# Optimization experiments

Hardware: AMD Instinct MI355X
Metric: run time of the kernel (lower is better)

The kernel has to match this reference:

```python
import jax, jax.numpy as jnp
from jax import lax
import numpy as np

VOCAB, EMB, HID, B, T = 500, 64, 64, 512, 512


def setup_inputs() -> dict:
    key = jax.random.key(0)
    ks = jax.random.split(key, 12)
    s_ih = 1.0 / np.sqrt(HID)
    emb = jax.random.normal(ks[0], (VOCAB, EMB), dtype=jnp.float32)
    emb = emb.at[0].set(0.0)  # padding_idx=0 row is zero-initialized
    u = lambda k, shape: jax.random.uniform(k, shape, jnp.float32, -s_ih, s_ih)
    return {
        "x": jax.random.randint(ks[1], (B, T), 0, VOCAB, dtype=jnp.int64),
        "emb": emb,
        "W_ih0": u(ks[2], (HID, EMB)), "W_hh0": u(ks[3], (HID, HID)),
        "b_ih0": u(ks[4], (HID,)),     "b_hh0": u(ks[5], (HID,)),
        "W_ih1": u(ks[6], (HID, HID)), "W_hh1": u(ks[7], (HID, HID)),
        "b_ih1": u(ks[8], (HID,)),     "b_hh1": u(ks[9], (HID,)),
        "fc_w": u(ks[10], (1, HID)),   "fc_b": u(ks[11], (1,)),
    }


def reference(x, emb, W_ih0, W_hh0, b_ih0, b_hh0, W_ih1, W_hh1, b_ih1, b_hh1, fc_w, fc_b):
    e = emb[x]                                        # [B,T,EMB]
    # Layer-0 input projection is time-parallel; precompute as one big GEMM.
    xin0 = jnp.einsum('bte,he->bth', e, W_ih0) + b_ih0  # [B,T,HID]

    def step(carry, xt):
        h1, h2 = carry
        h1 = jnp.tanh(xt + h1 @ W_hh0.T + b_hh0)
        h2 = jnp.tanh(h1 @ W_ih1.T + b_ih1 + h2 @ W_hh1.T + b_hh1)
        return (h1, h2), None

    h0 = jnp.zeros((x.shape[0], HID), dtype=e.dtype)
    (h1, h2), _ = lax.scan(step, (h0, h0), jnp.swapaxes(xin0, 0, 1))  # scan over T
    return h2 @ fc_w.T + fc_b                          # [B,1]
```

## Files before the change

### kernel.cpp

```cpp
#include <hip/hip_runtime.h>
#include <math.h>

#define VOCAB 500
#define EMB   64
#define HID   64
#define BB    512
#define TT    512

__device__ __forceinline__ float fast_tanh(float x) {
    float ax = fabsf(x);
    float e  = __expf(-2.0f * ax);
    float r  = __builtin_amdgcn_rcpf(1.0f + e);
    float t  = fmaf(-2.0f * e, r, 1.0f);
    return copysignf(t, x);
}

__global__ __launch_bounds__(64) void proj_kernel(
        const float* __restrict__ emb,
        const float* __restrict__ W_ih0,
        const float* __restrict__ b_ih0,
        float* __restrict__ proj) {
    const int v = blockIdx.x;
    const int j = threadIdx.x;
    const float4* e4 = (const float4*)(emb + v * EMB);
    const float4* w4 = (const float4*)(W_ih0 + j * EMB);
    float acc = b_ih0[j];
    #pragma unroll
    for (int k = 0; k < EMB / 4; ++k) {
        float4 e = e4[k];
        float4 w = w4[k];
        acc = fmaf(w.x, e.x, acc);
        acc = fmaf(w.y, e.y, acc);
        acc = fmaf(w.z, e.z, acc);
        acc = fmaf(w.w, e.w, acc);
    }
    proj[v * HID + j] = acc;
}

__global__ __launch_bounds__(192, 1) void rnn_kernel(
        const int*   __restrict__ x,
        const float* __restrict__ proj,
        const float* __restrict__ W_hh0,
        const float* __restrict__ b_hh0,
        const float* __restrict__ W_ih1,
        const float* __restrict__ W_hh1,
        const float* __restrict__ b_ih1,
        const float* __restrict__ b_hh1,
        const float* __restrict__ fc_w,
        const float* __restrict__ fc_b,
        float* __restrict__ out) {
    const int b   = blockIdx.x;
    const int tid = threadIdx.x;
    const int wid = tid >> 6;
    const int j   = tid & 63;

    __shared__ __align__(16) float H1[2][HID];
    __shared__ __align__(16) float H2[2][HID];
    __shared__ __align__(16) float AA[2][HID];
    __shared__ int xls[TT];

    for (int t = tid; t < TT; t += 192) xls[t] = x[b * TT + t];

    const float* wsrc = (wid == 0 ? W_hh0 : (wid == 1 ? W_ih1 : W_hh1)) + j * HID;
    float w[HID];
    {
        const float4* w4 = (const float4*)wsrc;
        #pragma unroll
        for (int k = 0; k < HID / 4; ++k) {
            float4 t4 = w4[k];
            w[4*k+0] = t4.x; w[4*k+1] = t4.y; w[4*k+2] = t4.z; w[4*k+3] = t4.w;
        }
    }
    #pragma unroll
    for (int k = 0; k < HID; ++k) asm volatile("" : "+v"(w[k]));

    const float bh0 = b_hh0[j];
    const float bi1 = b_ih1[j] + b_hh1[j];
    const float fcw = fc_w[j];

    if (tid < HID) {
        H1[0][tid] = 0.0f; H1[1][tid] = 0.0f;
        H2[0][tid] = 0.0f; H2[1][tid] = 0.0f;
    }
    __syncthreads();

    float xin = (wid == 0) ? proj[xls[0] * HID + j] : 0.0f;
    float h2n = 0.0f;

    for (int p = 0; p < TT + 2; ++p) {
        const int cur = p & 1;
        const int prv = cur ^ 1;

        if (wid == 0) {
            if (p < TT) {
                const int   idxn = xls[(p + 1) & (TT - 1)];
                const float xinn = proj[idxn * HID + j];

                const float4* h = (const float4*)H1[prv];
                float p0 = xin + bh0, p1 = 0.0f, p2 = 0.0f, p3 = 0.0f;
                #pragma unroll
                for (int k = 0; k < HID / 4; ++k) {
                    float4 hv = h[k];
                    p0 = fmaf(w[4*k+0], hv.x, p0);
                    p1 = fmaf(w[4*k+1], hv.y, p1);
                    p2 = fmaf(w[4*k+2], hv.z, p2);
                    p3 = fmaf(w[4*k+3], hv.w, p3);
                }
                H1[cur][j] = fast_tanh((p0 + p1) + (p2 + p3));
                xin = xinn;
            }
        } else if (wid == 1) {
            if (p >= 1 && p <= TT) {
                const float4* h = (const float4*)H1[prv];
                float p0 = 0.0f, p1 = 0.0f, p2 = 0.0f, p3 = 0.0f;
                #pragma unroll
                for (int k = 0; k < HID / 4; ++k) {
                    float4 hv = h[k];
                    p0 = fmaf(w[4*k+0], hv.x, p0);
                    p1 = fmaf(w[4*k+1], hv.y, p1);
                    p2 = fmaf(w[4*k+2], hv.z, p2);
                    p3 = fmaf(w[4*k+3], hv.w, p3);
                }
                AA[prv][j] = (p0 + p1) + (p2 + p3);
            }
        } else {
            if (p >= 2) {
                const float4* h = (const float4*)H2[prv];
                float p0 = bi1 + AA[cur][j], p1 = 0.0f, p2 = 0.0f, p3 = 0.0f;
                #pragma unroll
                for (int k = 0; k < HID / 4; ++k) {
                    float4 hv = h[k];
                    p0 = fmaf(w[4*k+0], hv.x, p0);
                    p1 = fmaf(w[4*k+1], hv.y, p1);
                    p2 = fmaf(w[4*k+2], hv.z, p2);
                    p3 = fmaf(w[4*k+3], hv.w, p3);
                }
                h2n = fast_tanh((p0 + p1) + (p2 + p3));
                H2[cur][j] = h2n;
            }
        }
        __syncthreads();
    }

    if (wid == 2) {
        float val = h2n * fcw;
        #pragma unroll
        for (int o = 32; o > 0; o >>= 1) val += __shfl_down(val, o, 64);
        if (j == 0) out[b] = val + fc_b[0];
    }
}

extern "C" void kernel_launch(void* const* d_in, const int* in_sizes, int n_in,
                              void* d_out, int out_size, void* d_ws, size_t ws_size,
                              hipStream_t stream) {
    const int*   x     = (const int*)  d_in[0];
    const float* emb   = (const float*)d_in[1];
    const float* W_ih0 = (const float*)d_in[2];
    const float* W_hh0 = (const float*)d_in[3];
    const float* b_ih0 = (const float*)d_in[4];
    const float* b_hh0 = (const float*)d_in[5];
    const float* W_ih1 = (const float*)d_in[6];
    const float* W_hh1 = (const float*)d_in[7];
    const float* b_ih1 = (const float*)d_in[8];
    const float* b_hh1 = (const float*)d_in[9];
    const float* fc_w  = (const float*)d_in[10];
    const float* fc_b  = (const float*)d_in[11];
    float* out  = (float*)d_out;
    float* proj = (float*)d_ws;

    proj_kernel<<<VOCAB, 64, 0, stream>>>(emb, W_ih0, b_ih0, proj);
    rnn_kernel<<<BB, 192, 0, stream>>>(x, proj, W_hh0, b_hh0,
                                       W_ih1, W_hh1, b_ih1, b_hh1,
                                       fc_w, fc_b, out);
}
```

Baseline: 323.2 us.

## Chunk recurrence by 8 steps with readlane broadcasts to cut block barriers

Each wave now handles 8 timesteps per barrier instead of one. The two recurrent waves keep their hidden state in a register and broadcast it with readlane rather than reading it back from shared memory. Layer-1 input products pass through chunked double-buffered shared arrays. This cuts __syncthreads from one per timestep to one per chunk and removes LDS round-trips on the serial critical path. In exchange it uses 64 scalar readlanes per step and adds a longer pipeline fill across the three waves.

```diff
diff --git a/kernel.cpp b/kernel.cpp
--- a/kernel.cpp
+++ b/kernel.cpp
@@ -6,6 +6,8 @@
 #define HID   64
 #define BB    512
 #define TT    512
+#define KC    8
+#define NC    (TT / KC)
 
 __device__ __forceinline__ float fast_tanh(float x) {
     float ax = fabsf(x);
@@ -13,6 +15,10 @@
     float r  = __builtin_amdgcn_rcpf(1.0f + e);
     float t  = fmaf(-2.0f * e, r, 1.0f);
     return copysignf(t, x);
+}
+
+__device__ __forceinline__ float bcast(float v, int lane) {
+    return __int_as_float(__builtin_amdgcn_readlane(__float_as_int(v), lane));
 }
 
 __global__ __launch_bounds__(64) void proj_kernel(
@@ -54,9 +60,8 @@
     const int wid = tid >> 6;
     const int j   = tid & 63;
 
-    __shared__ __align__(16) float H1[2][HID];
-    __shared__ __align__(16) float H2[2][HID];
-    __shared__ __align__(16) float AA[2][HID];
+    __shared__ __align__(16) float H1R[2][KC][HID];
+    __shared__ __align__(16) float AAR[2][KC][HID];
     __shared__ int xls[TT];
 
     for (int t = tid; t < TT; t += 192) xls[t] = x[b * TT + t];
@@ -78,72 +83,78 @@
     const float bi1 = b_ih1[j] + b_hh1[j];
     const float fcw = fc_w[j];
 
-    if (tid < HID) {
-        H1[0][tid] = 0.0f; H1[1][tid] = 0.0f;
-        H2[0][tid] = 0.0f; H2[1][tid] = 0.0f;
-    }
     __syncthreads();
 
-    float xin = (wid == 0) ? proj[xls[0] * HID + j] : 0.0f;
-    float h2n = 0.0f;
+    float h1reg = 0.0f, h2reg = 0.0f;
+    float xin[KC], xinN[KC];
+    if (wid == 0) {
+        #pragma unroll
+        for (int u = 0; u < KC; ++u) xin[u] = proj[xls[u] * HID + j];
+    }
 
-    for (int p = 0; p < TT + 2; ++p) {
-        const int cur = p & 1;
-        const int prv = cur ^ 1;
+    for (int c = 0; c < NC + 2; ++c) {
+        if (wid == 0) {
+            if (c < NC) {
+                const int base = ((c + 1) & (NC - 1)) * KC;
+                #pragma unroll
+                for (int u = 0; u < KC; ++u)
+                    xinN[u] = proj[xls[base + u] * HID + j];
 
-        if (wid == 0) {
-            if (p < TT) {
-                const int   idxn = xls[(p + 1) & (TT - 1)];
-                const float xinn = proj[idxn * HID + j];
-
-                const float4* h = (const float4*)H1[prv];
-                float p0 = xin + bh0, p1 = 0.0f, p2 = 0.0f, p3 = 0.0f;
                 #pragma unroll
-                for (int k = 0; k < HID / 4; ++k) {
-                    float4 hv = h[k];
-                    p0 = fmaf(w[4*k+0], hv.x, p0);
-                    p1 = fmaf(w[4*k+1], hv.y, p1);
-                    p2 = fmaf(w[4*k+2], hv.z, p2);
-                    p3 = fmaf(w[4*k+3], hv.w, p3);
+                for (int u = 0; u < KC; ++u) {
+                    float a0 = xin[u] + bh0, a1 = 0.0f, a2 = 0.0f, a3 = 0.0f;
+                    #pragma unroll
+                    for (int k = 0; k < HID; k += 4) {
+                        a0 = fmaf(w[k+0], bcast(h1reg, k+0), a0);
+                        a1 = fmaf(w[k+1], bcast(h1reg, k+1), a1);
+                        a2 = fmaf(w[k+2], bcast(h1reg, k+2), a2);
+                        a3 = fmaf(w[k+3], bcast(h1reg, k+3), a3);
+                    }
+                    h1reg = fast_tanh((a0 + a1) + (a2 + a3));
+                    H1R[c & 1][u][j] = h1reg;
+                    xin[u] = xinN[u];
                 }
-                H1[cur][j] = fast_tanh((p0 + p1) + (p2 + p3));
-                xin = xinn;
             }
         } else if (wid == 1) {
-            if (p >= 1 && p <= TT) {
-                const float4* h = (const float4*)H1[prv];
-                float p0 = 0.0f, p1 = 0.0f, p2 = 0.0f, p3 = 0.0f;
+            if (c >= 1 && c <= NC) {
+                const int p = (c - 1) & 1;
                 #pragma unroll
-                for (int k = 0; k < HID / 4; ++k) {
-                    float4 hv = h[k];
-                    p0 = fmaf(w[4*k+0], hv.x, p0);
-                    p1 = fmaf(w[4*k+1], hv.y, p1);
-                    p2 = fmaf(w[4*k+2], hv.z, p2);
-                    p3 = fmaf(w[4*k+3], hv.w, p3);
+                for (int u = 0; u < KC; ++u) {
+                    const float4* hv = (const float4*)(&H1R[p][u][0]);
+                    float a0 = 0.0f, a1 = 0.0f, a2 = 0.0f, a3 = 0.0f;
+                    #pragma unroll
+                    for (int k = 0; k < HID / 4; ++k) {
+                        float4 h = hv[k];
+                        a0 = fmaf(w[4*k+0], h.x, a0);
+                        a1 = fmaf(w[4*k+1], h.y, a1);
+                        a2 = fmaf(w[4*k+2], h.z, a2);
+                        a3 = fmaf(w[4*k+3], h.w, a3);
+                    }
+                    AAR[p][u][j] = (a0 + a1) + (a2 + a3);
                 }
-                AA[prv][j] = (p0 + p1) + (p2 + p3);
             }
         } else {
-            if (p >= 2) {
-                const float4* h = (const float4*)H2[prv];
-                float p0 = bi1 + AA[cur][j], p1 = 0.0f, p2 = 0.0f, p3 = 0.0f;
+            if (c >= 2) {
+                const int p = c & 1;
                 #pragma unroll
-                for (int k = 0; k < HID / 4; ++k) {
-                    float4 hv = h[k];
-                    p0 = fmaf(w[4*k+0], hv.x, p0);
-                    p1 = fmaf(w[4*k+1], hv.y, p1);
-                    p2 = fmaf(w[4*k+2], hv.z, p2);
-                    p3 = fmaf(w[4*k+3], hv.w, p3);
+                for (int u = 0; u < KC; ++u) {
+                    float a0 = AAR[p][u][j] + bi1, a1 = 0.0f, a2 = 0.0f, a3 = 0.0f;
+                    #pragma unroll
+                    for (int k = 0; k < HID; k += 4) {
+                        a0 = fmaf(w[k+0], bcast(h2reg, k+0), a0);
+                        a1 = fmaf(w[k+1], bcast(h2reg, k+1), a1);
+                        a2 = fmaf(w[k+2], bcast(h2reg, k+2), a2);
+                        a3 = fmaf(w[k+3], bcast(h2reg, k+3), a3);
+                    }
+                    h2reg = fast_tanh((a0 + a1) + (a2 + a3));
                 }
-                h2n = fast_tanh((p0 + p1) + (p2 + p3));
-                H2[cur][j] = h2n;
             }
         }
         __syncthreads();
     }
 
     if (wid == 2) {
-        float val = h2n * fcw;
+        float val = h2reg * fcw;
         #pragma unroll
         for (int o = 32; o > 0; o >>= 1) val += __shfl_down(val, o, 64);
         if (j == 0) out[b] = val + fc_b[0];
```

Measured after the change: 318.4 us. About the same (-1.5%).
